# Kernel tuning notes

Hardware: AMD Instinct MI355X
Metric: run time of the kernel (lower is better)

The kernel has to match this reference:

```python
import jax, jax.numpy as jnp
import numpy as np
from jax import lax

# mamba-130m-hf config
N_LAYERS = 24
D_MODEL = 768
D_INNER = 1536   # expand=2
D_STATE = 16
DT_RANK = 48     # ceil(768/16)
D_CONV = 4
VOCAB = 50280
ENC_DIM = 256
EPS = 1e-5
SEQ, BATCH = 512, 2  # input is (SEQ, BATCH, ENC_DIM); permute -> mamba batch=BATCH, seq=SEQ


def setup_inputs() -> dict:
    key = jax.random.key(0)
    ks = jax.random.split(key, 12)
    f = jnp.float32
    def rn(k, shape, scale=0.02):
        return (jax.random.normal(k, shape) * scale).astype(f)
    x = jax.random.normal(ks[0], (SEQ, BATCH, ENC_DIM), dtype=f)
    W_et = rn(ks[1], (D_MODEL, ENC_DIM))
    b_et = jnp.zeros((D_MODEL,), f)
    in_proj_w = rn(ks[2], (N_LAYERS, 2 * D_INNER, D_MODEL))
    conv_w = rn(ks[3], (N_LAYERS, D_INNER, D_CONV), 0.1)
    conv_b = jnp.zeros((N_LAYERS, D_INNER), f)
    x_proj_w = rn(ks[4], (N_LAYERS, DT_RANK + 2 * D_STATE, D_INNER))
    dt_proj_w = rn(ks[5], (N_LAYERS, D_INNER, DT_RANK), 0.1)
    # bias init so softplus(bias) lands in [1e-3, 1e-1] (standard mamba dt init)
    dt_init = jnp.exp(jax.random.uniform(ks[6], (N_LAYERS, D_INNER), minval=jnp.log(1e-3), maxval=jnp.log(1e-1)))
    dt_proj_b = jnp.log(jnp.expm1(dt_init)).astype(f)
    A_log = jnp.log(jnp.broadcast_to(jnp.arange(1, D_STATE + 1, dtype=f), (N_LAYERS, D_INNER, D_STATE))) * jnp.ones((1,), f)
    D = jnp.ones((N_LAYERS, D_INNER), f)
    out_proj_w = rn(ks[7], (N_LAYERS, D_MODEL, D_INNER))
    norm_w = jnp.ones((N_LAYERS, D_MODEL), f)
    final_norm_w = jnp.ones((D_MODEL,), f)
    embed = rn(ks[8], (VOCAB, D_MODEL))
    return {"x": x, "W_et": W_et, "b_et": b_et, "in_proj_w": in_proj_w, "conv_w": conv_w,
            "conv_b": conv_b, "x_proj_w": x_proj_w, "dt_proj_w": dt_proj_w, "dt_proj_b": dt_proj_b,
            "A_log": A_log, "D": D, "out_proj_w": out_proj_w, "norm_w": norm_w,
            "final_norm_w": final_norm_w, "embed": embed}


def rmsnorm(x, w):
    return x * lax.rsqrt(jnp.mean(x * x, axis=-1, keepdims=True) + EPS) * w


def mamba_layer(h, p):
    in_w, cw, cb, xw, dtw, dtb, Al, Dv, ow, nw = p
    hn = rmsnorm(h, nw)
    xz = hn @ in_w.T                       # (B,T,2*D_INNER)
    xi, z = jnp.split(xz, 2, axis=-1)
    # depthwise causal conv over time
    xc = lax.conv_general_dilated(xi.transpose(0, 2, 1), cw[:, None, :], (1,),
                                  [(D_CONV - 1, 0)], dimension_numbers=("NCH", "OIH", "NCH"),
                                  feature_group_count=D_INNER)
    xc = jax.nn.silu(xc + cb[None, :, None]).transpose(0, 2, 1)   # (B,T,D_INNER)
    proj = xc @ xw.T                                              # (B,T,DT_RANK+2*D_STATE)
    dt = jax.nn.softplus(proj[..., :DT_RANK] @ dtw.T + dtb)       # (B,T,D_INNER)
    Bm = proj[..., DT_RANK:DT_RANK + D_STATE]                     # (B,T,S)
    Cm = proj[..., DT_RANK + D_STATE:]                            # (B,T,S)
    A = -jnp.exp(Al)                                              # (D_INNER,S)
    dA = jnp.exp(dt[..., None] * A)                               # (B,T,D,S)
    dBx = dt[..., None] * Bm[:, :, None, :] * xc[..., None]       # (B,T,D,S)

    def step(hst, inp):
        a, bx, c = inp
        hst = a * hst + bx
        return hst, jnp.einsum("bds,bs->bd", hst, c)

    h0 = jnp.zeros(dA.shape[:1] + dA.shape[2:], dA.dtype)
    _, ys = lax.scan(step, h0, (dA.transpose(1, 0, 2, 3), dBx.transpose(1, 0, 2, 3), Cm.transpose(1, 0, 2)))
    y = ys.transpose(1, 0, 2) + Dv * xc
    y = y * jax.nn.silu(z)
    return h + y @ ow.T


def reference(x, W_et, b_et, in_proj_w, conv_w, conv_b, x_proj_w, dt_proj_w, dt_proj_b,
              A_log, D, out_proj_w, norm_w, final_norm_w, embed):
    h = (x @ W_et.T + b_et).transpose(1, 0, 2)   # permute(1,0,2): (B,T,D_MODEL)

    def body(hc, p):
        return mamba_layer(hc, p), None

    h, _ = lax.scan(body, h, (in_proj_w, conv_w, conv_b, x_proj_w, dt_proj_w,
                              dt_proj_b, A_log, D, out_proj_w, norm_w))
    h = rmsnorm(h, final_norm_w)
    return h @ embed.T                            # tied lm_head logits (B,T,VOCAB)
```

## Files before the change

### kernel.cpp

```cpp
#include <hip/hip_runtime.h>
#include <math.h>

#define N_LAYERS 24
#define D_MODEL 768
#define D_INNER 1536
#define D_STATE 16
#define DT_RANK 48
#define D_CONV 4
#define VOCAB 50280
#define ENC_DIM 256
#define SEQ 512
#define BATCH 2
#define NTOK (SEQ*BATCH)
#define XZ_DIM (2*D_INNER)
#define PROJ_DIM (DT_RANK + 2*D_STATE)
#define DTW_PAD 64
#define XP_SPLIT 8
#define OP_SPLIT 4

typedef __attribute__((ext_vector_type(8))) short bf16x8;
typedef __attribute__((ext_vector_type(4))) float f32x4;

__device__ __forceinline__ float sigmoidf_(float x) { return 1.f / (1.f + __expf(-x)); }
__device__ __forceinline__ float softplusf_(float x) {
    return fmaxf(x, 0.f) + log1pf(__expf(-fabsf(x)));
}
__device__ __forceinline__ short f2bf(float f) {
    unsigned u = __float_as_uint(f);
    unsigned r = (u + 0x7FFFu + ((u >> 16) & 1u)) >> 16;
    return (short)r;
}
__device__ __forceinline__ void load_lds16(const void* g, void* l) {
    __builtin_amdgcn_global_load_lds((const __attribute__((address_space(1))) void*)g,
                                     (__attribute__((address_space(3))) void*)l, 16, 0, 0);
}

__global__ __launch_bounds__(256) void cvt_k(const float* __restrict__ s,
                                             short* __restrict__ d, int n) {
    int stride = gridDim.x * 256 * 4;
    for (int i = (blockIdx.x * 256 + threadIdx.x) * 4; i + 3 < n; i += stride) {
        float4 f = *(const float4*)(s + i);
        short4 o; o.x = f2bf(f.x); o.y = f2bf(f.y); o.z = f2bf(f.z); o.w = f2bf(f.w);
        *(short4*)(d + i) = o;
    }
}

__global__ __launch_bounds__(256) void pad_dtw_k(const float* __restrict__ src,
                                                 short* __restrict__ dst) {
    int i = blockIdx.x * 256 + threadIdx.x;
    if (i >= N_LAYERS * D_INNER * DTW_PAD) return;
    int k = i & (DTW_PAD - 1);
    int rest = i >> 6;
    dst[i] = (k < DT_RANK) ? f2bf(src[(size_t)rest * DT_RANK + k]) : (short)0;
}

__global__ __launch_bounds__(256) void transpose_x_k(const float* __restrict__ x,
                                                     float* __restrict__ xt) {
    int i = blockIdx.x * 256 + threadIdx.x;
    if (i >= SEQ * BATCH * ENC_DIM) return;
    int e = i % ENC_DIM;
    int b = (i / ENC_DIM) % BATCH;
    int l = i / (ENC_DIM * BATCH);
    xt[((size_t)(b * SEQ + l)) * ENC_DIM + e] = x[i];
}
__global__ __launch_bounds__(256) void transpose_x_bf_k(const float* __restrict__ x,
                                                        short* __restrict__ xt) {
    int i = blockIdx.x * 256 + threadIdx.x;
    if (i >= SEQ * BATCH * ENC_DIM) return;
    int e = i % ENC_DIM;
    int b = (i / ENC_DIM) % BATCH;
    int l = i / (ENC_DIM * BATCH);
    xt[((size_t)(b * SEQ + l)) * ENC_DIM + e] = f2bf(x[i]);
}

__device__ __forceinline__ float rms_scale(const float* r, int tid) {
    float s = 0.f;
    for (int i = tid; i < D_MODEL; i += 256) { float v = r[i]; s += v * v; }
    for (int o = 32; o > 0; o >>= 1) s += __shfl_down(s, o);
    __shared__ float wsum[4];
    if ((tid & 63) == 0) wsum[tid >> 6] = s;
    __syncthreads();
    float tot = wsum[0] + wsum[1] + wsum[2] + wsum[3];
    return rsqrtf(tot / (float)D_MODEL + 1e-5f);
}
__global__ __launch_bounds__(256) void rmsnorm_k(const float* __restrict__ in,
                                                 const float* __restrict__ w,
                                                 float* __restrict__ out) {
    int row = blockIdx.x;
    const float* r = in + (size_t)row * D_MODEL;
    float sc = rms_scale(r, threadIdx.x);
    for (int i = threadIdx.x; i < D_MODEL; i += 256)
        out[(size_t)row * D_MODEL + i] = r[i] * sc * w[i];
}
__global__ __launch_bounds__(256) void rmsnorm_bf_k(const float* __restrict__ in,
                                                    const float* __restrict__ w,
                                                    short* __restrict__ out) {
    int row = blockIdx.x;
    const float* r = in + (size_t)row * D_MODEL;
    float sc = rms_scale(r, threadIdx.x);
    for (int i = threadIdx.x; i < D_MODEL; i += 256)
        out[(size_t)row * D_MODEL + i] = f2bf(r[i] * sc * w[i]);
}

template<int MODE, int BM, int DEPTH>
__global__ __launch_bounds__(256)
void gemm_p2(const short* __restrict__ A, const short* __restrict__ B,
             const float* __restrict__ bias, float* __restrict__ C,
             short* __restrict__ Cb,
             int M, int N, int K, int ldaE, int ldbE, int ldc, int ldcb)
{
    constexpr int NBUF = DEPTH + 1;
    constexpr int MI = BM / 32;
    constexpr int AELEM = 4 * BM;
    constexpr int BELEM = 4 * 128;
    constexpr int LA = AELEM / 256;
    constexpr int LB = BELEM / 256;
    constexpr int L = LA + LB;
    __shared__ short lA[NBUF][AELEM * 8];
    __shared__ short lB[NBUF][BELEM * 8];

    const int nx = gridDim.x;
    int lin = blockIdx.y * nx + blockIdx.x;
    const int nwg = nx * gridDim.y;
    if ((nwg & 7) == 0) { const int cpx = nwg >> 3; lin = (lin & 7) * cpx + (lin >> 3); }
    const int bm = (lin % nx) * BM;
    const int bn = (lin / nx) * 128;
    const int koff = blockIdx.z * K;

    const int t = threadIdx.x;
    const int wave = t >> 6;
    const int wm = (wave >> 1) * (BM / 2), wn = (wave & 1) * 64;
    const int l15 = t & 15, l4 = (t & 63) >> 4;

    f32x4 acc[MI][4] = {};
    const int nkt = K / 32;

    auto stage = [&](int buf, int kt) {
        const int k0 = koff + kt * 32;
        #pragma unroll
        for (int u = 0; u < LA; ++u) {
            const int idx = t + u * 256;
            const int kg = idx / BM;
            const int row = idx % BM;
            load_lds16(A + (size_t)(bm + row) * ldaE + k0 + kg * 8,
                       &lA[buf][(wave * 64 + u * 256) * 8]);
        }
        #pragma unroll
        for (int u = 0; u < LB; ++u) {
            const int idx = t + u * 256;
            const int kg = idx >> 7;
            const int row = idx & 127;
            int brow = bn + row; if (brow >= N) brow = 0;
            load_lds16(B + (size_t)brow * ldbE + k0 + kg * 8,
                       &lB[buf][(wave * 64 + u * 256) * 8]);
        }
    };

    #pragma unroll
    for (int p = 0; p < DEPTH; ++p)
        if (p < nkt) stage(p, p);

    for (int kt = 0; kt < nkt; ++kt) {
        const int rem = nkt - 1 - kt;
        const int ahead = rem < (DEPTH - 1) ? rem : (DEPTH - 1);
        if (ahead == 2) {
            if constexpr (L == 3) asm volatile("s_waitcnt vmcnt(6)" ::: "memory");
            else                  asm volatile("s_waitcnt vmcnt(8)" ::: "memory");
        } else if (ahead == 1) {
            if constexpr (L == 3) asm volatile("s_waitcnt vmcnt(3)" ::: "memory");
            else                  asm volatile("s_waitcnt vmcnt(4)" ::: "memory");
        } else {
            asm volatile("s_waitcnt vmcnt(0)" ::: "memory");
        }
        __builtin_amdgcn_s_barrier();
        __builtin_amdgcn_sched_barrier(0);
        if (kt + DEPTH < nkt) stage((kt + DEPTH) % NBUF, kt + DEPTH);
        const int cbuf = kt % NBUF;
        const short* bA = lA[cbuf];
        const short* bB = lB[cbuf];
        bf16x8 af[MI], bfr[4];
        #pragma unroll
        for (int i = 0; i < MI; ++i)
            af[i] = *(const bf16x8*)&bA[(l4 * BM + wm + i * 16 + l15) * 8];
        #pragma unroll
        for (int j = 0; j < 4; ++j)
            bfr[j] = *(const bf16x8*)&bB[(l4 * 128 + wn + j * 16 + l15) * 8];
        #pragma unroll
        for (int i = 0; i < MI; ++i)
            #pragma unroll
            for (int j = 0; j < 4; ++j)
                acc[i][j] = __builtin_amdgcn_mfma_f32_16x16x32_bf16(
                    af[i], bfr[j], acc[i][j], 0, 0, 0);
    }

    float* Cp = (MODE == 5) ? C + (size_t)blockIdx.z * M * ldc : C;
    #pragma unroll
    for (int i = 0; i < MI; ++i) {
        #pragma unroll
        for (int r = 0; r < 4; ++r) {
            const int row = bm + wm + i * 16 + l4 * 4 + r;
            #pragma unroll
            for (int j = 0; j < 4; ++j) {
                const int col = bn + wn + j * 16 + l15;
                if (col < N) {
                    float v = acc[i][j][r];
                    if (MODE == 1) v += bias[col];
                    if (MODE == 2) v = softplusf_(v + bias[col]);
                    if (MODE == 3) v += C[(size_t)row * ldc + col];
                    Cp[(size_t)row * ldc + col] = v;
                    if (MODE == 4) Cb[(size_t)row * ldcb + col] = f2bf(v);
                }
            }
        }
    }
}

__global__ __launch_bounds__(256) void reduce_xp_k(const float* __restrict__ part,
                                                   float* __restrict__ proj,
                                                   short* __restrict__ projb) {
    const int n4 = NTOK * PROJ_DIM / 4;
    int i = blockIdx.x * 256 + threadIdx.x;
    if (i >= n4) return;
    float4 s = ((const float4*)part)[i];
    #pragma unroll
    for (int p = 1; p < XP_SPLIT; ++p) {
        float4 v = ((const float4*)part)[i + p * n4];
        s.x += v.x; s.y += v.y; s.z += v.z; s.w += v.w;
    }
    ((float4*)proj)[i] = s;
    short4 o; o.x = f2bf(s.x); o.y = f2bf(s.y); o.z = f2bf(s.z); o.w = f2bf(s.w);
    ((short4*)projb)[i] = o;
}
__global__ __launch_bounds__(256) void reduce_out_k(const float* __restrict__ part,
                                                    float* __restrict__ h) {
    const int n4 = NTOK * D_MODEL / 4;
    int i = blockIdx.x * 256 + threadIdx.x;
    if (i >= n4) return;
    float4 s = ((const float4*)h)[i];
    #pragma unroll
    for (int p = 0; p < OP_SPLIT; ++p) {
        float4 v = ((const float4*)part)[i + p * n4];
        s.x += v.x; s.y += v.y; s.z += v.z; s.w += v.w;
    }
    ((float4*)h)[i] = s;
}

template<int MODE>
__global__ __launch_bounds__(256)
void gemm_bf16(const float* __restrict__ A, const float* __restrict__ B,
               const float* __restrict__ bias, float* __restrict__ C,
               int M, int N, int K, int lda, int ldb, int ldc)
{
    __shared__ short lA[4 * 128 * 8];
    __shared__ short lB[4 * 128 * 8];
    const int bm = blockIdx.x * 128;
    const int bn = blockIdx.y * 128;
    const int t = threadIdx.x;
    const int wave = t >> 6, lane = t & 63;
    const int wm = (wave >> 1) * 64, wn = (wave & 1) * 64;
    const int l15 = lane & 15, l4 = lane >> 4;
    const int row2 = t >> 1;
    const int khalf = (t & 1) * 16;
    const int kgbase = khalf >> 3;
    f32x4 acc[4][4] = {};
    const int nkt = (K + 31) / 32;
    for (int kt = 0; kt < nkt; ++kt) {
        const int k0 = kt * 32 + khalf;
        {
            short v[16];
            const float* src = A + (size_t)(bm + row2) * lda + k0;
            if (k0 + 16 <= K) {
                #pragma unroll
                for (int j = 0; j < 16; j += 4) {
                    float4 f = *(const float4*)(src + j);
                    v[j+0]=f2bf(f.x); v[j+1]=f2bf(f.y); v[j+2]=f2bf(f.z); v[j+3]=f2bf(f.w);
                }
            } else {
                #pragma unroll
                for (int j = 0; j < 16; ++j)
                    v[j] = (k0 + j < K) ? f2bf(src[j]) : (short)0;
            }
            short* dst = &lA[(kgbase * 128 + row2) * 8];
            *(bf16x8*)dst = *(const bf16x8*)&v[0];
            *(bf16x8*)(dst + 128 * 8) = *(const bf16x8*)&v[8];
        }
        {
            short v[16];
            const int nrow = bn + row2;
            if (nrow < N) {
                const float* src = B + (size_t)nrow * ldb + k0;
                if (k0 + 16 <= K) {
                    #pragma unroll
                    for (int j = 0; j < 16; j += 4) {
                        float4 f = *(const float4*)(src + j);
                        v[j+0]=f2bf(f.x); v[j+1]=f2bf(f.y); v[j+2]=f2bf(f.z); v[j+3]=f2bf(f.w);
                    }
                } else {
                    #pragma unroll
                    for (int j = 0; j < 16; ++j)
                        v[j] = (k0 + j < K) ? f2bf(src[j]) : (short)0;
                }
            } else {
                #pragma unroll
                for (int j = 0; j < 16; ++j) v[j] = 0;
            }
            short* dst = &lB[(kgbase * 128 + row2) * 8];
            *(bf16x8*)dst = *(const bf16x8*)&v[0];
            *(bf16x8*)(dst + 128 * 8) = *(const bf16x8*)&v[8];
        }
        __syncthreads();
        bf16x8 af[4], bfr[4];
        #pragma unroll
        for (int i = 0; i < 4; ++i)
            af[i] = *(const bf16x8*)&lA[(l4 * 128 + wm + i * 16 + l15) * 8];
        #pragma unroll
        for (int j = 0; j < 4; ++j)
            bfr[j] = *(const bf16x8*)&lB[(l4 * 128 + wn + j * 16 + l15) * 8];
        #pragma unroll
        for (int i = 0; i < 4; ++i)
            #pragma unroll
            for (int j = 0; j < 4; ++j)
                acc[i][j] = __builtin_amdgcn_mfma_f32_16x16x32_bf16(
                    af[i], bfr[j], acc[i][j], 0, 0, 0);
        __syncthreads();
    }
    #pragma unroll
    for (int i = 0; i < 4; ++i) {
        #pragma unroll
        for (int r = 0; r < 4; ++r) {
            const int row = bm + wm + i * 16 + l4 * 4 + r;
            #pragma unroll
            for (int j = 0; j < 4; ++j) {
                const int col = bn + wn + j * 16 + l15;
                if (col < N) {
                    float v = acc[i][j][r];
                    if (MODE == 1) v += bias[col];
                    if (MODE == 2) v = softplusf_(v + bias[col]);
                    if (MODE == 3) v += C[(size_t)row * ldc + col];
                    C[(size_t)row * ldc + col] = v;
                }
            }
        }
    }
}

template<int DUAL>
__global__ __launch_bounds__(256) void conv_silu_k(const float* __restrict__ xz,
                                                   const float* __restrict__ cw,
                                                   const float* __restrict__ cb,
                                                   float* __restrict__ xc,
                                                   short* __restrict__ xcb) {
    int idx = blockIdx.x * 256 + threadIdx.x;
    if (idx >= NTOK * D_INNER) return;
    int d = idx % D_INNER;
    int m = idx / D_INNER;
    int l = m % SEQ;
    int b = m / SEQ;
    float acc = cb[d];
    #pragma unroll
    for (int j = 0; j < D_CONV; ++j) {
        int ll = l - (D_CONV - 1) + j;
        if (ll >= 0)
            acc = fmaf(cw[d * D_CONV + j], xz[(size_t)(b * SEQ + ll) * XZ_DIM + d], acc);
    }
    float v = acc * sigmoidf_(acc);
    xc[(size_t)m * D_INNER + d] = v;
    if (DUAL) xcb[(size_t)m * D_INNER + d] = f2bf(v);
}

#define SCAN_DW 16
#define SCAN_NC 32
#define SCAN_CL (SEQ / SCAN_NC)
template<int BFOUT>
__global__ __launch_bounds__(512) void scan3_k(const float* __restrict__ proj,
                                               const float* __restrict__ dtb,
                                               const float* __restrict__ xc,
                                               const float* __restrict__ xz,
                                               const float* __restrict__ A_log,
                                               const float* __restrict__ Dvec,
                                               void* __restrict__ yout) {
    __shared__ float lp[D_STATE][SCAN_NC][SCAN_DW];
    __shared__ float ls[D_STATE][SCAN_NC][SCAN_DW];
    const int nblk_d = D_INNER / SCAN_DW;
    const int b  = blockIdx.x / nblk_d;
    const int d0 = (blockIdx.x % nblk_d) * SCAN_DW;
    const int t  = threadIdx.x;
    const int dl = t & (SCAN_DW - 1);
    const int c  = t >> 4;
    const int d  = d0 + dl;

    float A[D_STATE];
    #pragma unroll
    for (int s = 0; s < D_STATE; s += 4) {
        float4 a4 = *(const float4*)&A_log[(size_t)d * D_STATE + s];
        A[s+0] = -__expf(a4.x); A[s+1] = -__expf(a4.y);
        A[s+2] = -__expf(a4.z); A[s+3] = -__expf(a4.w);
    }
    const int m0 = b * SEQ + c * SCAN_CL;

    float P[D_STATE], S[D_STATE];
    #pragma unroll
    for (int s = 0; s < D_STATE; ++s) { P[s] = 1.f; S[s] = 0.f; }
    for (int i = 0; i < SCAN_CL; ++i) {
        const int m = m0 + i;
        float dtv = dtb[(size_t)m * D_INNER + d];
        float xcv = xc[(size_t)m * D_INNER + d];
        float dx = dtv * xcv;
        const float* pB = proj + (size_t)m * PROJ_DIM + DT_RANK;
        float Bv[D_STATE];
        #pragma unroll
        for (int s = 0; s < D_STATE; s += 4)
            *(float4*)&Bv[s] = *(const float4*)(pB + s);
        #pragma unroll
        for (int s = 0; s < D_STATE; ++s) {
            float da = __expf(dtv * A[s]);
            S[s] = fmaf(da, S[s], dx * Bv[s]);
            P[s] *= da;
        }
    }
    #pragma unroll
    for (int s = 0; s < D_STATE; ++s) { lp[s][c][dl] = P[s]; ls[s][c][dl] = S[s]; }
    __syncthreads();

    float st[D_STATE];
    #pragma unroll
    for (int s = 0; s < D_STATE; ++s) st[s] = 0.f;
    for (int j = 0; j < c; ++j) {
        #pragma unroll
        for (int s = 0; s < D_STATE; ++s)
            st[s] = fmaf(lp[s][j][dl], st[s], ls[s][j][dl]);
    }

    const float Dvv = Dvec[d];
    for (int i = 0; i < SCAN_CL; ++i) {
        const int m = m0 + i;
        float dtv = dtb[(size_t)m * D_INNER + d];
        float xcv = xc[(size_t)m * D_INNER + d];
        float dx = dtv * xcv;
        const float* pB = proj + (size_t)m * PROJ_DIM + DT_RANK;
        float Bv[D_STATE], Cv[D_STATE];
        #pragma unroll
        for (int s = 0; s < D_STATE; s += 4) {
            *(float4*)&Bv[s] = *(const float4*)(pB + s);
            *(float4*)&Cv[s] = *(const float4*)(pB + D_STATE + s);
        }
        float acc = Dvv * xcv;
        #pragma unroll
        for (int s = 0; s < D_STATE; ++s) {
            float da = __expf(dtv * A[s]);
            st[s] = fmaf(da, st[s], dx * Bv[s]);
            acc = fmaf(st[s], Cv[s], acc);
        }
        float zv = xz[(size_t)m * XZ_DIM + D_INNER + d];
        float yv = acc * (zv * sigmoidf_(zv));
        if (BFOUT) ((short*)yout)[(size_t)m * D_INNER + d] = f2bf(yv);
        else       ((float*)yout)[(size_t)m * D_INNER + d] = yv;
    }
}

extern "C" void kernel_launch(void* const* d_in, const int* in_sizes, int n_in,
                              void* d_out, int out_size, void* d_ws, size_t ws_size,
                              hipStream_t stream) {
    const float* x           = (const float*)d_in[0];
    const float* W_et        = (const float*)d_in[1];
    const float* b_et        = (const float*)d_in[2];
    const float* in_proj_w   = (const float*)d_in[3];
    const float* conv_w      = (const float*)d_in[4];
    const float* conv_b      = (const float*)d_in[5];
    const float* x_proj_w    = (const float*)d_in[6];
    const float* dt_proj_w   = (const float*)d_in[7];
    const float* dt_proj_b   = (const float*)d_in[8];
    const float* A_log       = (const float*)d_in[9];
    const float* Dv          = (const float*)d_in[10];
    const float* out_proj_w  = (const float*)d_in[11];
    const float* norm_w      = (const float*)d_in[12];
    const float* final_norm_w= (const float*)d_in[13];
    const float* embed       = (const float*)d_in[14];
    float* out = (float*)d_out;
    float* ws  = (float*)d_ws;

    float* h    = ws;
    float* hn   = h    + (size_t)NTOK * D_MODEL;
    float* xz   = hn   + (size_t)NTOK * D_MODEL;
    float* xc   = xz   + (size_t)NTOK * XZ_DIM;
    float* proj = xc   + (size_t)NTOK * D_INNER;
    float* dt   = proj + (size_t)NTOK * PROJ_DIM;
    float* yb   = dt   + (size_t)NTOK * D_INNER;
    short* xt_bf   = (short*)(yb + (size_t)NTOK * D_INNER);
    short* hn_bf   = xt_bf   + (size_t)NTOK * ENC_DIM;
    short* xc_bf   = hn_bf   + (size_t)NTOK * D_MODEL;
    short* proj_bf = xc_bf   + (size_t)NTOK * D_INNER;
    short* yb_bf   = proj_bf + (size_t)NTOK * PROJ_DIM;
    short* wet_bf  = yb_bf   + (size_t)NTOK * D_INNER;
    short* inw_bf  = wet_bf  + (size_t)D_MODEL * ENC_DIM;
    short* xw_bf   = inw_bf  + (size_t)N_LAYERS * XZ_DIM * D_MODEL;
    short* dtw_bf  = xw_bf   + (size_t)N_LAYERS * PROJ_DIM * D_INNER;
    short* ow_bf   = dtw_bf  + (size_t)N_LAYERS * D_INNER * DTW_PAD;
    short* emb_bf  = ow_bf   + (size_t)N_LAYERS * D_MODEL * D_INNER;
    short* end_bf  = emb_bf  + (size_t)VOCAB * D_MODEL;
    size_t needA = (size_t)((char*)end_bf - (char*)d_ws);
    bool tierA = ws_size >= needA;

    dim3 blk(256);
    const int scan_blocks = BATCH * (D_INNER / SCAN_DW);

    if (tierA) {
        auto cvt = [&](const float* s, short* d, size_t n) {
            int nb = (int)((n / 4 + 255) / 256); if (nb > 2048) nb = 2048;
            cvt_k<<<nb, blk, 0, stream>>>(s, d, (int)n);
        };
        cvt(W_et, wet_bf, (size_t)D_MODEL * ENC_DIM);
        cvt(in_proj_w, inw_bf, (size_t)N_LAYERS * XZ_DIM * D_MODEL);
        cvt(x_proj_w, xw_bf, (size_t)N_LAYERS * PROJ_DIM * D_INNER);
        cvt(out_proj_w, ow_bf, (size_t)N_LAYERS * D_MODEL * D_INNER);
        cvt(embed, emb_bf, (size_t)VOCAB * D_MODEL);
        pad_dtw_k<<<(N_LAYERS * D_INNER * DTW_PAD + 255) / 256, blk, 0, stream>>>(
            dt_proj_w, dtw_bf);

        transpose_x_bf_k<<<(SEQ * BATCH * ENC_DIM + 255) / 256, blk, 0, stream>>>(x, xt_bf);
        gemm_p2<1, 64, 2><<<dim3(NTOK / 64, D_MODEL / 128), blk, 0, stream>>>(
            xt_bf, wet_bf, b_et, h, nullptr,
            NTOK, D_MODEL, ENC_DIM, ENC_DIM, ENC_DIM, D_MODEL, 0);

        for (int L = 0; L < N_LAYERS; ++L) {
            const short* in_w = inw_bf + (size_t)L * XZ_DIM * D_MODEL;
            const float* cw   = conv_w + (size_t)L * D_INNER * D_CONV;
            const float* cb   = conv_b + (size_t)L * D_INNER;
            const short* xw   = xw_bf  + (size_t)L * PROJ_DIM * D_INNER;
            const short* dtw  = dtw_bf + (size_t)L * D_INNER * DTW_PAD;
            const float* dtbp = dt_proj_b + (size_t)L * D_INNER;
            const float* Al   = A_log  + (size_t)L * D_INNER * D_STATE;
            const float* Dl   = Dv     + (size_t)L * D_INNER;
            const short* ow   = ow_bf  + (size_t)L * D_MODEL * D_INNER;
            const float* nw   = norm_w + (size_t)L * D_MODEL;

            rmsnorm_bf_k<<<NTOK, blk, 0, stream>>>(h, nw, hn_bf);
            gemm_p2<0, 64, 3><<<dim3(NTOK / 64, XZ_DIM / 128), blk, 0, stream>>>(
                hn_bf, in_w, nullptr, xz, nullptr,
                NTOK, XZ_DIM, D_MODEL, D_MODEL, D_MODEL, XZ_DIM, 0);
            conv_silu_k<1><<<(NTOK * D_INNER + 255) / 256, blk, 0, stream>>>(
                xz, cw, cb, xc, xc_bf);
            gemm_p2<5, 64, 3><<<dim3(NTOK / 64, 1, XP_SPLIT), blk, 0, stream>>>(
                xc_bf, xw, nullptr, hn, nullptr,
                NTOK, PROJ_DIM, D_INNER / XP_SPLIT, D_INNER, D_INNER, PROJ_DIM, 0);
            reduce_xp_k<<<(NTOK * PROJ_DIM / 4 + 255) / 256, blk, 0, stream>>>(
                hn, proj, proj_bf);
            gemm_p2<2, 64, 2><<<dim3(NTOK / 64, D_INNER / 128), blk, 0, stream>>>(
                proj_bf, dtw, dtbp, dt, nullptr,
                NTOK, D_INNER, DTW_PAD, PROJ_DIM, DTW_PAD, D_INNER, 0);
            scan3_k<1><<<scan_blocks, dim3(512), 0, stream>>>(
                proj, dt, xc, xz, Al, Dl, yb_bf);
            gemm_p2<5, 64, 3><<<dim3(NTOK / 64, D_MODEL / 128, OP_SPLIT), blk, 0, stream>>>(
                yb_bf, ow, nullptr, xz, nullptr,
                NTOK, D_MODEL, D_INNER / OP_SPLIT, D_INNER, D_INNER, D_MODEL, 0);
            reduce_out_k<<<(NTOK * D_MODEL / 4 + 255) / 256, blk, 0, stream>>>(
                xz, h);
        }

        rmsnorm_bf_k<<<NTOK, blk, 0, stream>>>(h, final_norm_w, hn_bf);
        gemm_p2<0, 128, 2><<<dim3(NTOK / 128, (VOCAB + 127) / 128), blk, 0, stream>>>(
            hn_bf, emb_bf, nullptr, out, nullptr,
            NTOK, VOCAB, D_MODEL, D_MODEL, D_MODEL, VOCAB, 0);
    } else {
        transpose_x_k<<<(SEQ * BATCH * ENC_DIM + 255) / 256, blk, 0, stream>>>(x, yb);
        gemm_bf16<1><<<dim3(NTOK / 128, D_MODEL / 128), blk, 0, stream>>>(
            yb, W_et, b_et, h, NTOK, D_MODEL, ENC_DIM, ENC_DIM, ENC_DIM, D_MODEL);
        for (int L = 0; L < N_LAYERS; ++L) {
            const float* in_w = in_proj_w  + (size_t)L * XZ_DIM * D_MODEL;
            const float* cw   = conv_w     + (size_t)L * D_INNER * D_CONV;
            const float* cb   = conv_b     + (size_t)L * D_INNER;
            const float* xw   = x_proj_w   + (size_t)L * PROJ_DIM * D_INNER;
            const float* dtw  = dt_proj_w  + (size_t)L * D_INNER * DT_RANK;
            const float* dtbp = dt_proj_b  + (size_t)L * D_INNER;
            const float* Al   = A_log      + (size_t)L * D_INNER * D_STATE;
            const float* Dl   = Dv         + (size_t)L * D_INNER;
            const float* ow   = out_proj_w + (size_t)L * D_MODEL * D_INNER;
            const float* nw   = norm_w     + (size_t)L * D_MODEL;
            rmsnorm_k<<<NTOK, blk, 0, stream>>>(h, nw, hn);
            gemm_bf16<0><<<dim3(NTOK / 128, XZ_DIM / 128), blk, 0, stream>>>(
                hn, in_w, nullptr, xz, NTOK, XZ_DIM, D_MODEL, D_MODEL, D_MODEL, XZ_DIM);
            conv_silu_k<0><<<(NTOK * D_INNER + 255) / 256, blk, 0, stream>>>(
                xz, cw, cb, xc, nullptr);
            gemm_bf16<0><<<dim3(NTOK / 128, 1), blk, 0, stream>>>(
                xc, xw, nullptr, proj, NTOK, PROJ_DIM, D_INNER, D_INNER, D_INNER, PROJ_DIM);
            gemm_bf16<2><<<dim3(NTOK / 128, D_INNER / 128), blk, 0, stream>>>(
                proj, dtw, dtbp, dt, NTOK, D_INNER, DT_RANK, PROJ_DIM, DT_RANK, D_INNER);
            scan3_k<0><<<scan_blocks, dim3(512), 0, stream>>>(
                proj, dt, xc, xz, Al, Dl, yb);
            gemm_bf16<3><<<dim3(NTOK / 128, D_MODEL / 128), blk, 0, stream>>>(
                yb, ow, nullptr, h, NTOK, D_MODEL, D_INNER, D_INNER, D_INNER, D_MODEL);
        }
        rmsnorm_k<<<NTOK, blk, 0, stream>>>(h, final_norm_w, hn);
        gemm_bf16<0><<<dim3(NTOK / 128, (VOCAB + 127) / 128), blk, 0, stream>>>(
            hn, embed, nullptr, out, NTOK, VOCAB, D_MODEL, D_MODEL, D_MODEL, VOCAB);
    }
}
```

Before: 3.168 ms.

## Fuse split-K reductions with conv and rmsnorm, store intermediates in bf16

The in_proj GEMM now uses split-K with two partials. Its reduction is fused with the causal conv and SiLU, and the kernel writes bf16 xc and z directly. The out_proj reduction is fused with the next layer's RMSNorm, which removes a separate rmsnorm launch per layer. dt is written as bf16 from a new softplus epilogue mode, and the scan reads bf16 dt, xc and z, which cuts memory traffic. The cost is extra rounding of dt, xc and z to bf16, plus redundant partial reads in the conv reduction.

```diff
diff --git a/kernel.cpp b/kernel.cpp
--- a/kernel.cpp
+++ b/kernel.cpp
@@ -15,6 +15,7 @@
 #define XZ_DIM (2*D_INNER)
 #define PROJ_DIM (DT_RANK + 2*D_STATE)
 #define DTW_PAD 64
+#define IN_SPLIT 2
 #define XP_SPLIT 8
 #define OP_SPLIT 4
 
@@ -29,6 +30,9 @@
     unsigned u = __float_as_uint(f);
     unsigned r = (u + 0x7FFFu + ((u >> 16) & 1u)) >> 16;
     return (short)r;
+}
+__device__ __forceinline__ float bf2f(short s) {
+    return __uint_as_float(((unsigned)(unsigned short)s) << 16);
 }
 __device__ __forceinline__ void load_lds16(const void* g, void* l) {
     __builtin_amdgcn_global_load_lds((const __attribute__((address_space(1))) void*)g,
@@ -204,14 +208,50 @@
                 const int col = bn + wn + j * 16 + l15;
                 if (col < N) {
                     float v = acc[i][j][r];
-                    if (MODE == 1) v += bias[col];
-                    if (MODE == 2) v = softplusf_(v + bias[col]);
-                    if (MODE == 3) v += C[(size_t)row * ldc + col];
-                    Cp[(size_t)row * ldc + col] = v;
-                    if (MODE == 4) Cb[(size_t)row * ldcb + col] = f2bf(v);
+                    if (MODE == 6) {
+                        Cb[(size_t)row * ldcb + col] = f2bf(softplusf_(v + bias[col]));
+                    } else {
+                        if (MODE == 1) v += bias[col];
+                        if (MODE == 2) v = softplusf_(v + bias[col]);
+                        if (MODE == 3) v += C[(size_t)row * ldc + col];
+                        Cp[(size_t)row * ldc + col] = v;
+                        if (MODE == 4) Cb[(size_t)row * ldcb + col] = f2bf(v);
+                    }
                 }
             }
         }
+    }
+}
+
+__global__ __launch_bounds__(256) void reduce_conv_k(const float* __restrict__ part,
+                                                     const float* __restrict__ cw,
+                                                     const float* __restrict__ cb,
+                                                     short* __restrict__ xcb,
+                                                     short* __restrict__ zb) {
+    int idx = blockIdx.x * 256 + threadIdx.x;
+    if (idx >= NTOK * XZ_DIM) return;
+    int d3 = idx % XZ_DIM;
+    int m  = idx / XZ_DIM;
+    if (d3 < D_INNER) {
+        int l = m % SEQ;
+        float acc = cb[d3];
+        #pragma unroll
+        for (int j = 0; j < D_CONV; ++j) {
+            int ll = l - (D_CONV - 1) + j;
+            if (ll >= 0) {
+                int mm = m - (D_CONV - 1) + j;
+                float v = part[(size_t)mm * XZ_DIM + d3]
+                        + part[(size_t)(NTOK + mm) * XZ_DIM + d3];
+                acc = fmaf(cw[d3 * D_CONV + j], v, acc);
+            }
+        }
+        float v = acc * sigmoidf_(acc);
+        xcb[(size_t)m * D_INNER + d3] = f2bf(v);
+    } else {
+        int d = d3 - D_INNER;
+        float z = part[(size_t)m * XZ_DIM + d3]
+                + part[(size_t)(NTOK + m) * XZ_DIM + d3];
+        zb[(size_t)m * D_INNER + d] = f2bf(z);
     }
 }
 
@@ -231,18 +271,37 @@
     short4 o; o.x = f2bf(s.x); o.y = f2bf(s.y); o.z = f2bf(s.z); o.w = f2bf(s.w);
     ((short4*)projb)[i] = o;
 }
-__global__ __launch_bounds__(256) void reduce_out_k(const float* __restrict__ part,
-                                                    float* __restrict__ h) {
-    const int n4 = NTOK * D_MODEL / 4;
-    int i = blockIdx.x * 256 + threadIdx.x;
-    if (i >= n4) return;
-    float4 s = ((const float4*)h)[i];
-    #pragma unroll
-    for (int p = 0; p < OP_SPLIT; ++p) {
-        float4 v = ((const float4*)part)[i + p * n4];
-        s.x += v.x; s.y += v.y; s.z += v.z; s.w += v.w;
-    }
-    ((float4*)h)[i] = s;
+
+__global__ __launch_bounds__(256) void reduce_rms_k(const float* __restrict__ part,
+                                                    float* __restrict__ h,
+                                                    const float* __restrict__ w,
+                                                    short* __restrict__ hnb) {
+    const int row = blockIdx.x;
+    const int i = threadIdx.x;
+    float4 s = make_float4(0.f, 0.f, 0.f, 0.f);
+    if (i < 192) {
+        s = ((const float4*)h)[row * 192 + i];
+        #pragma unroll
+        for (int p = 0; p < OP_SPLIT; ++p) {
+            float4 v = ((const float4*)part)[((size_t)p * NTOK + row) * 192 + i];
+            s.x += v.x; s.y += v.y; s.z += v.z; s.w += v.w;
+        }
+        ((float4*)h)[row * 192 + i] = s;
+    }
+    float ss = s.x * s.x + s.y * s.y + s.z * s.z + s.w * s.w;
+    for (int o = 32; o > 0; o >>= 1) ss += __shfl_down(ss, o);
+    __shared__ float wsum[4];
+    if ((i & 63) == 0) wsum[i >> 6] = ss;
+    __syncthreads();
+    float tot = wsum[0] + wsum[1] + wsum[2] + wsum[3];
+    float sc = rsqrtf(tot / (float)D_MODEL + 1e-5f);
+    if (i < 192) {
+        float4 w4 = ((const float4*)w)[i];
+        short4 o4;
+        o4.x = f2bf(s.x * sc * w4.x); o4.y = f2bf(s.y * sc * w4.y);
+        o4.z = f2bf(s.z * sc * w4.z); o4.w = f2bf(s.w * sc * w4.w);
+        ((short4*)hnb)[row * 192 + i] = o4;
+    }
 }
 
 template<int MODE>
@@ -355,13 +414,13 @@
     int d = idx % D_INNER;
     int m = idx / D_INNER;
     int l = m % SEQ;
-    int b = m / SEQ;
     float acc = cb[d];
     #pragma unroll
     for (int j = 0; j < D_CONV; ++j) {
         int ll = l - (D_CONV - 1) + j;
         if (ll >= 0)
-            acc = fmaf(cw[d * D_CONV + j], xz[(size_t)(b * SEQ + ll) * XZ_DIM + d], acc);
+            acc = fmaf(cw[d * D_CONV + j],
+                       xz[(size_t)(m - (D_CONV - 1) + j) * XZ_DIM + d], acc);
     }
     float v = acc * sigmoidf_(acc);
     xc[(size_t)m * D_INNER + d] = v;
@@ -371,11 +430,12 @@
 #define SCAN_DW 16
 #define SCAN_NC 32
 #define SCAN_CL (SEQ / SCAN_NC)
-template<int BFOUT>
+template<int BF>
 __global__ __launch_bounds__(512) void scan3_k(const float* __restrict__ proj,
-                                               const float* __restrict__ dtb,
-                                               const float* __restrict__ xc,
-                                               const float* __restrict__ xz,
+                                               const void* __restrict__ dtp,
+                                               const void* __restrict__ xcp,
+                                               const void* __restrict__ zp,
+                                               int zld,
                                                const float* __restrict__ A_log,
                                                const float* __restrict__ Dvec,
                                                void* __restrict__ yout) {
@@ -403,8 +463,14 @@
     for (int s = 0; s < D_STATE; ++s) { P[s] = 1.f; S[s] = 0.f; }
     for (int i = 0; i < SCAN_CL; ++i) {
         const int m = m0 + i;
-        float dtv = dtb[(size_t)m * D_INNER + d];
-        float xcv = xc[(size_t)m * D_INNER + d];
+        float dtv, xcv;
+        if (BF) {
+            dtv = bf2f(((const short*)dtp)[(size_t)m * D_INNER + d]);
+            xcv = bf2f(((const short*)xcp)[(size_t)m * D_INNER + d]);
+        } else {
+            dtv = ((const float*)dtp)[(size_t)m * D_INNER + d];
+            xcv = ((const float*)xcp)[(size_t)m * D_INNER + d];
+        }
         float dx = dtv * xcv;
         const float* pB = proj + (size_t)m * PROJ_DIM + DT_RANK;
         float Bv[D_STATE];
@@ -434,8 +500,16 @@
     const float Dvv = Dvec[d];
     for (int i = 0; i < SCAN_CL; ++i) {
         const int m = m0 + i;
-        float dtv = dtb[(size_t)m * D_INNER + d];
-        float xcv = xc[(size_t)m * D_INNER + d];
+        float dtv, xcv, zv;
+        if (BF) {
+            dtv = bf2f(((const short*)dtp)[(size_t)m * D_INNER + d]);
+            xcv = bf2f(((const short*)xcp)[(size_t)m * D_INNER + d]);
+            zv  = bf2f(((const short*)zp)[(size_t)m * zld + d]);
+        } else {
+            dtv = ((const float*)dtp)[(size_t)m * D_INNER + d];
+            xcv = ((const float*)xcp)[(size_t)m * D_INNER + d];
+            zv  = ((const float*)zp)[(size_t)m * zld + d];
+        }
         float dx = dtv * xcv;
         const float* pB = proj + (size_t)m * PROJ_DIM + DT_RANK;
         float Bv[D_STATE], Cv[D_STATE];
@@ -451,10 +525,9 @@
             st[s] = fmaf(da, st[s], dx * Bv[s]);
             acc = fmaf(st[s], Cv[s], acc);
         }
-        float zv = xz[(size_t)m * XZ_DIM + D_INNER + d];
         float yv = acc * (zv * sigmoidf_(zv));
-        if (BFOUT) ((short*)yout)[(size_t)m * D_INNER + d] = f2bf(yv);
-        else       ((float*)yout)[(size_t)m * D_INNER + d] = yv;
+        if (BF) ((short*)yout)[(size_t)m * D_INNER + d] = f2bf(yv);
+        else    ((float*)yout)[(size_t)m * D_INNER + d] = yv;
     }
 }
 
@@ -479,17 +552,15 @@
     float* out = (float*)d_out;
     float* ws  = (float*)d_ws;
 
-    float* h    = ws;
-    float* hn   = h    + (size_t)NTOK * D_MODEL;
-    float* xz   = hn   + (size_t)NTOK * D_MODEL;
-    float* xc   = xz   + (size_t)NTOK * XZ_DIM;
-    float* proj = xc   + (size_t)NTOK * D_INNER;
-    float* dt   = proj + (size_t)NTOK * PROJ_DIM;
-    float* yb   = dt   + (size_t)NTOK * D_INNER;
-    short* xt_bf   = (short*)(yb + (size_t)NTOK * D_INNER);
+    float* h       = ws;
+    float* proj    = h + (size_t)NTOK * D_MODEL;
+    float* scratch = proj + (size_t)NTOK * PROJ_DIM;
+    short* xt_bf   = (short*)(scratch + (size_t)IN_SPLIT * NTOK * XZ_DIM);
     short* hn_bf   = xt_bf   + (size_t)NTOK * ENC_DIM;
     short* xc_bf   = hn_bf   + (size_t)NTOK * D_MODEL;
-    short* proj_bf = xc_bf   + (size_t)NTOK * D_INNER;
+    short* z_bf    = xc_bf   + (size_t)NTOK * D_INNER;
+    short* dt_bf   = z_bf    + (size_t)NTOK * D_INNER;
+    short* proj_bf = dt_bf   + (size_t)NTOK * D_INNER;
     short* yb_bf   = proj_bf + (size_t)NTOK * PROJ_DIM;
     short* wet_bf  = yb_bf   + (size_t)NTOK * D_INNER;
     short* inw_bf  = wet_bf  + (size_t)D_MODEL * ENC_DIM;
@@ -521,6 +592,7 @@
         gemm_p2<1, 64, 2><<<dim3(NTOK / 64, D_MODEL / 128), blk, 0, stream>>>(
             xt_bf, wet_bf, b_et, h, nullptr,
             NTOK, D_MODEL, ENC_DIM, ENC_DIM, ENC_DIM, D_MODEL, 0);
+        rmsnorm_bf_k<<<NTOK, blk, 0, stream>>>(h, norm_w, hn_bf);
 
         for (int L = 0; L < N_LAYERS; ++L) {
             const short* in_w = inw_bf + (size_t)L * XZ_DIM * D_MODEL;
@@ -532,39 +604,45 @@
             const float* Al   = A_log  + (size_t)L * D_INNER * D_STATE;
             const float* Dl   = Dv     + (size_t)L * D_INNER;
             const short* ow   = ow_bf  + (size_t)L * D_MODEL * D_INNER;
-            const float* nw   = norm_w + (size_t)L * D_MODEL;
-
-            rmsnorm_bf_k<<<NTOK, blk, 0, stream>>>(h, nw, hn_bf);
-            gemm_p2<0, 64, 3><<<dim3(NTOK / 64, XZ_DIM / 128), blk, 0, stream>>>(
-                hn_bf, in_w, nullptr, xz, nullptr,
-                NTOK, XZ_DIM, D_MODEL, D_MODEL, D_MODEL, XZ_DIM, 0);
-            conv_silu_k<1><<<(NTOK * D_INNER + 255) / 256, blk, 0, stream>>>(
-                xz, cw, cb, xc, xc_bf);
+            const float* nw_next = (L == N_LAYERS - 1) ? final_norm_w
+                                 : norm_w + (size_t)(L + 1) * D_MODEL;
+
+            gemm_p2<5, 64, 3><<<dim3(NTOK / 64, XZ_DIM / 128, IN_SPLIT), blk, 0, stream>>>(
+                hn_bf, in_w, nullptr, scratch, nullptr,
+                NTOK, XZ_DIM, D_MODEL / IN_SPLIT, D_MODEL, D_MODEL, XZ_DIM, 0);
+            reduce_conv_k<<<(NTOK * XZ_DIM + 255) / 256, blk, 0, stream>>>(
+                scratch, cw, cb, xc_bf, z_bf);
             gemm_p2<5, 64, 3><<<dim3(NTOK / 64, 1, XP_SPLIT), blk, 0, stream>>>(
-                xc_bf, xw, nullptr, hn, nullptr,
+                xc_bf, xw, nullptr, scratch, nullptr,
                 NTOK, PROJ_DIM, D_INNER / XP_SPLIT, D_INNER, D_INNER, PROJ_DIM, 0);
             reduce_xp_k<<<(NTOK * PROJ_DIM / 4 + 255) / 256, blk, 0, stream>>>(
-                hn, proj, proj_bf);
-            gemm_p2<2, 64, 2><<<dim3(NTOK / 64, D_INNER / 128), blk, 0, stream>>>(
-                proj_bf, dtw, dtbp, dt, nullptr,
-                NTOK, D_INNER, DTW_PAD, PROJ_DIM, DTW_PAD, D_INNER, 0);
+                scratch, proj, proj_bf);
+            gemm_p2<6, 64, 2><<<dim3(NTOK / 64, D_INNER / 128), blk, 0, stream>>>(
+                proj_bf, dtw, dtbp, h , dt_bf,
+                NTOK, D_INNER, DTW_PAD, PROJ_DIM, DTW_PAD, D_INNER, D_INNER);
             scan3_k<1><<<scan_blocks, dim3(512), 0, stream>>>(
-                proj, dt, xc, xz, Al, Dl, yb_bf);
+                proj, dt_bf, xc_bf, z_bf, D_INNER, Al, Dl, yb_bf);
             gemm_p2<5, 64, 3><<<dim3(NTOK / 64, D_MODEL / 128, OP_SPLIT), blk, 0, stream>>>(
-                yb_bf, ow, nullptr, xz, nullptr,
+                yb_bf, ow, nullptr, scratch, nullptr,
                 NTOK, D_MODEL, D_INNER / OP_SPLIT, D_INNER, D_INNER, D_MODEL, 0);
-            reduce_out_k<<<(NTOK * D_MODEL / 4 + 255) / 256, blk, 0, stream>>>(
-                xz, h);
-        }
-
-        rmsnorm_bf_k<<<NTOK, blk, 0, stream>>>(h, final_norm_w, hn_bf);
+            reduce_rms_k<<<NTOK, blk, 0, stream>>>(scratch, h, nw_next, hn_bf);
+        }
+
         gemm_p2<0, 128, 2><<<dim3(NTOK / 128, (VOCAB + 127) / 128), blk, 0, stream>>>(
             hn_bf, emb_bf, nullptr, out, nullptr,
             NTOK, VOCAB, D_MODEL, D_MODEL, D_MODEL, VOCAB, 0);
     } else {
-        transpose_x_k<<<(SEQ * BATCH * ENC_DIM + 255) / 256, blk, 0, stream>>>(x, yb);
+        float* hB   = ws;
+        float* hnB  = hB   + (size_t)NTOK * D_MODEL;
+        float* xzB  = hnB  + (size_t)NTOK * D_MODEL;
+        float* xcB  = xzB  + (size_t)NTOK * XZ_DIM;
+        float* projB= xcB  + (size_t)NTOK * D_INNER;
+        float* dtB  = projB+ (size_t)NTOK * PROJ_DIM;
+        float* ybB  = dtB  + (size_t)NTOK * D_INNER;
+
+        transpose_x_k<<<(SEQ * BATCH * ENC_DIM + 255) / 256, blk, 0, stream>>>(x, ybB);
         gemm_bf16<1><<<dim3(NTOK / 128, D_MODEL / 128), blk, 0, stream>>>(
-            yb, W_et, b_et, h, NTOK, D_MODEL, ENC_DIM, ENC_DIM, ENC_DIM, D_MODEL);
+            ybB, W_et, b_et, hB, NTOK, D_MODEL, ENC_DIM, ENC_DIM, ENC_DIM, D_MODEL);
         for (int L = 0; L < N_LAYERS; ++L) {
             const float* in_w = in_proj_w  + (size_t)L * XZ_DIM * D_MODEL;
             const float* cw   = conv_w     + (size_t)L * D_INNER * D_CONV;
@@ -576,22 +654,22 @@
             const float* Dl   = Dv         + (size_t)L * D_INNER;
             const float* ow   = out_proj_w + (size_t)L * D_MODEL * D_INNER;
             const float* nw   = norm_w     + (size_t)L * D_MODEL;
-            rmsnorm_k<<<NTOK, blk, 0, stream>>>(h, nw, hn);
+            rmsnorm_k<<<NTOK, blk, 0, stream>>>(hB, nw, hnB);
             gemm_bf16<0><<<dim3(NTOK / 128, XZ_DIM / 128), blk, 0, stream>>>(
-                hn, in_w, nullptr, xz, NTOK, XZ_DIM, D_MODEL, D_MODEL, D_MODEL, XZ_DIM);
+                hnB, in_w, nullptr, xzB, NTOK, XZ_DIM, D_MODEL, D_MODEL, D_MODEL, XZ_DIM);
             conv_silu_k<0><<<(NTOK * D_INNER + 255) / 256, blk, 0, stream>>>(
-                xz, cw, cb, xc, nullptr);
+                xzB, cw, cb, xcB, nullptr);
             gemm_bf16<0><<<dim3(NTOK / 128, 1), blk, 0, stream>>>(
-                xc, xw, nullptr, proj, NTOK, PROJ_DIM, D_INNER, D_INNER, D_INNER, PROJ_DIM);
+                xcB, xw, nullptr, projB, NTOK, PROJ_DIM, D_INNER, D_INNER, D_INNER, PROJ_DIM);
             gemm_bf16<2><<<dim3(NTOK / 128, D_INNER / 128), blk, 0, stream>>>(
-                proj, dtw, dtbp, dt, NTOK, D_INNER, DT_RANK, PROJ_DIM, DT_RANK, D_INNER);
+                projB, dtw, dtbp, dtB, NTOK, D_INNER, DT_RANK, PROJ_DIM, DT_RANK, D_INNER);
             scan3_k<0><<<scan_blocks, dim3(512), 0, stream>>>(
-                proj, dt, xc, xz, Al, Dl, yb);
+                projB, dtB, xcB, xzB + D_INNER, XZ_DIM, Al, Dl, ybB);
             gemm_bf16<3><<<dim3(NTOK / 128, D_MODEL / 128), blk, 0, stream>>>(
-                yb, ow, nullptr, h, NTOK, D_MODEL, D_INNER, D_INNER, D_INNER, D_MODEL);
-        }
-        rmsnorm_k<<<NTOK, blk, 0, stream>>>(h, final_norm_w, hn);
+                ybB, ow, nullptr, hB, NTOK, D_MODEL, D_INNER, D_INNER, D_INNER, D_MODEL);
+        }
+        rmsnorm_k<<<NTOK, blk, 0, stream>>>(hB, final_norm_w, hnB);
         gemm_bf16<0><<<dim3(NTOK / 128, (VOCAB + 127) / 128), blk, 0, stream>>>(
-            hn, embed, nullptr, out, NTOK, VOCAB, D_MODEL, D_MODEL, D_MODEL, VOCAB);
-    }
-}
+            hnB, embed, nullptr, out, NTOK, VOCAB, D_MODEL, D_MODEL, D_MODEL, VOCAB);
+    }
+}
```

After: 3.011 ms. -5.0%, faster.
